# Optimization experiments

Measured on AMD Instinct MI355X. Metric: run time of the kernel, lower is better.

The kernel has to match this reference:

```python
import jax, jax.numpy as jnp
import numpy as np

COMMITMENT_COST = 0.25
LAMBDA_KL = 1.0
EPS = 1e-10


def setup_inputs() -> dict:
    key = jax.random.key(0)
    k1, k2 = jax.random.split(key)
    x = jax.random.normal(k1, (8, 4096, 256), dtype=jnp.float32)
    embedding = jax.random.normal(k2, (1024, 256), dtype=jnp.float32)
    return {"x": x, "embedding": embedding}


def reference(x, embedding):
    B, T, D = x.shape
    M, _ = embedding.shape
    x_sg = jax.lax.stop_gradient(x)
    x_flat = x_sg.reshape(-1, D)  # [N, D]
    distances = (jnp.sum(embedding ** 2, axis=1)[None, :]
                 + jnp.sum(x_flat ** 2, axis=1, keepdims=True)
                 - 2.0 * (x_flat @ embedding.T))  # [N, M]
    indices = jnp.argmin(distances.astype(jnp.float32), axis=-1)  # [N]
    quantized = embedding[indices].reshape(B, T, D)
    # losses (x detached in both terms, matching torch)
    loss = (COMMITMENT_COST * jnp.mean((x_sg - quantized) ** 2)
            + jnp.mean((quantized - x_sg) ** 2)) * LAMBDA_KL
    # straight-through estimator
    quantized_st = x + jax.lax.stop_gradient(quantized - x)
    # avg of one-hot encodings == normalized code counts (avoids NxM one-hot)
    N = B * T
    counts = jnp.zeros((M,), dtype=jnp.float32).at[indices].add(1.0)
    avg_probs = counts / N
    perplexity = jnp.exp(-jnp.sum(avg_probs * jnp.log(avg_probs + EPS)))
    return (quantized_st, loss, indices.reshape(B, T), perplexity)
```

## Files before the change

### kernel.cpp

```cpp
#include <hip/hip_runtime.h>


constexpr int D = 256;
constexpr int M = 1024;
constexpr int ROWS = 64;

typedef _Float16 f16;
typedef __attribute__((ext_vector_type(8))) _Float16 f16x8;
typedef __attribute__((ext_vector_type(4))) float f32x4;

constexpr size_t WS_ENORM_F = 1028;
constexpr size_t WS_TAB_B   = 8320;
constexpr size_t WS_NEEDED  = 1056896;

__device__ inline void gload_lds16(const void* g, void* l) {
    __builtin_amdgcn_global_load_lds(
        (const __attribute__((address_space(1))) unsigned int*)(g),
        (__attribute__((address_space(3))) unsigned int*)(l), 16, 0, 0);
}

__global__ __launch_bounds__(256) void prep_kernel(const float* __restrict__ e,
                                                   float* __restrict__ ws) {
    const int b = blockIdx.x, t = threadIdx.x;
    if (b < 256) {
        int v    = b * 256 + t;
        int lane = v & 63, unit = v >> 6;
        int rf = unit & 1, spl = (unit >> 1) & 1, kk = (unit >> 2) & 7, tile = unit >> 5;
        int lr = lane & 15, q = lane >> 4;
        const float* p = e + (size_t)(tile * 32 + rf * 16 + lr) * D + kk * 32 + q * 8;
        f32x4 a = *reinterpret_cast<const f32x4*>(p);
        f32x4 c = *reinterpret_cast<const f32x4*>(p + 4);
        f16 h0=(f16)a.x,h1=(f16)a.y,h2=(f16)a.z,h3=(f16)a.w;
        f16 h4=(f16)c.x,h5=(f16)c.y,h6=(f16)c.z,h7=(f16)c.w;
        f16x8 out;
        if (spl == 0) out = (f16x8){h0,h1,h2,h3,h4,h5,h6,h7};
        else          out = (f16x8){(f16)(a.x-(float)h0),(f16)(a.y-(float)h1),
                                    (f16)(a.z-(float)h2),(f16)(a.w-(float)h3),
                                    (f16)(c.x-(float)h4),(f16)(c.y-(float)h5),
                                    (f16)(c.z-(float)h6),(f16)(c.w-(float)h7)};
        *reinterpret_cast<f16x8*>((char*)ws + WS_TAB_B + (size_t)v * 16) = out;
    } else {
        int row  = (b - 256) * 4 + (t >> 6);
        int lane = t & 63;
        f32x4 a = *reinterpret_cast<const f32x4*>(e + (size_t)row * D + lane * 4);
        float s = fmaf(a.x, a.x, fmaf(a.y, a.y, fmaf(a.z, a.z, a.w * a.w)));
#pragma unroll
        for (int o = 32; o > 0; o >>= 1) s += __shfl_down(s, o, 64);
        if (lane == 0) ws[WS_ENORM_F + row] = s;
    }
}

__global__ __launch_bounds__(256, 2) void vq_fused_kernel(
    const float* __restrict__ x, const float* __restrict__ e,
    float* __restrict__ outQ, float* __restrict__ outIdx, float* __restrict__ ws)
{
    __shared__ ushort ebuf[2][16384];
    __shared__ float  en_s[M];
    __shared__ int    fidx[ROWS];
    __shared__ float  lsum[4];

    const int tid = threadIdx.x;
    const int w   = __builtin_amdgcn_readfirstlane(tid >> 6);
    const int l   = tid & 63;
    const int lr  = l & 15, q = l >> 4;
    const int R   = blockIdx.x * ROWS;
    const char* tab = (const char*)ws + WS_TAB_B;

    {
        f32x4 v = *reinterpret_cast<const f32x4*>(ws + WS_ENORM_F + tid * 4);
        *reinterpret_cast<f32x4*>(&en_s[tid * 4]) = v;
    }

    f16x8 Xh[8], Xl[8];
    float xn;
    {
        float s = 0.f;
#pragma unroll
        for (int kk = 0; kk < 8; ++kk) {
            const float* p = x + (size_t)(R + w * 16 + lr) * D + kk * 32 + q * 8;
            f32x4 a = *reinterpret_cast<const f32x4*>(p);
            f32x4 c = *reinterpret_cast<const f32x4*>(p + 4);
            f16 h0=(f16)a.x,h1=(f16)a.y,h2=(f16)a.z,h3=(f16)a.w;
            f16 h4=(f16)c.x,h5=(f16)c.y,h6=(f16)c.z,h7=(f16)c.w;
            Xh[kk] = (f16x8){h0,h1,h2,h3,h4,h5,h6,h7};
            Xl[kk] = (f16x8){(f16)(a.x-(float)h0),(f16)(a.y-(float)h1),
                             (f16)(a.z-(float)h2),(f16)(a.w-(float)h3),
                             (f16)(c.x-(float)h4),(f16)(c.y-(float)h5),
                             (f16)(c.z-(float)h6),(f16)(c.w-(float)h7)};
            s = fmaf(a.x,a.x,fmaf(a.y,a.y,fmaf(a.z,a.z,fmaf(a.w,a.w,
                fmaf(c.x,c.x,fmaf(c.y,c.y,fmaf(c.z,c.z,fmaf(c.w,c.w,s))))))));
        }
        s += __shfl_xor(s, 16, 64);
        s += __shfl_xor(s, 32, 64);
        xn = s;
    }

#pragma unroll
    for (int i = 0; i < 8; ++i)
        gload_lds16(tab + (w * 8 + i) * 1024 + l * 16, &ebuf[0][(w * 8 + i) * 512]);
    __syncthreads();

    float bV = 3.4e38f;
    int   bI = 0;

    for (int t = 0; t < 32; ++t) {
        const ushort* eb = &ebuf[t & 1][0];
        if (t < 31) {
            const char* gt = tab + (size_t)(t + 1) * 32768;
            ushort* lb = &ebuf[(t + 1) & 1][0];
#pragma unroll
            for (int i = 0; i < 8; ++i)
                gload_lds16(gt + (w * 8 + i) * 1024 + l * 16, lb + (w * 8 + i) * 512);
        }

        f32x4 accA[2], accB[2];
#pragma unroll
        for (int rf = 0; rf < 2; ++rf) {
            accA[rf] = (f32x4){0.f,0.f,0.f,0.f};
            accB[rf] = (f32x4){0.f,0.f,0.f,0.f};
        }
#pragma unroll
        for (int kk = 0; kk < 8; ++kk) {
            f16x8 Ah0 = *reinterpret_cast<const f16x8*>(eb + (kk*4+0)*512 + l*8);
            f16x8 Ah1 = *reinterpret_cast<const f16x8*>(eb + (kk*4+1)*512 + l*8);
            f16x8 Al0 = *reinterpret_cast<const f16x8*>(eb + (kk*4+2)*512 + l*8);
            f16x8 Al1 = *reinterpret_cast<const f16x8*>(eb + (kk*4+3)*512 + l*8);
            accA[0] = __builtin_amdgcn_mfma_f32_16x16x32_f16(Ah0, Xh[kk], accA[0], 0, 0, 0);
            accA[0] = __builtin_amdgcn_mfma_f32_16x16x32_f16(Ah0, Xl[kk], accA[0], 0, 0, 0);
            accB[0] = __builtin_amdgcn_mfma_f32_16x16x32_f16(Al0, Xh[kk], accB[0], 0, 0, 0);
            accA[1] = __builtin_amdgcn_mfma_f32_16x16x32_f16(Ah1, Xh[kk], accA[1], 0, 0, 0);
            accA[1] = __builtin_amdgcn_mfma_f32_16x16x32_f16(Ah1, Xl[kk], accA[1], 0, 0, 0);
            accB[1] = __builtin_amdgcn_mfma_f32_16x16x32_f16(Al1, Xh[kk], accB[1], 0, 0, 0);
        }
        __syncthreads();

#pragma unroll
        for (int rf = 0; rf < 2; ++rf) {
            f32x4 en4 = *reinterpret_cast<const f32x4*>(&en_s[t * 32 + rf * 16 + q * 4]);
#pragma unroll
            for (int i = 0; i < 4; ++i) {
                float dv = fmaf(-2.f, accA[rf][i] + accB[rf][i], en4[i]);
                int   mi = t * 32 + rf * 16 + q * 4 + i;
                if (dv < bV) { bV = dv; bI = mi; }
            }
        }
    }

#pragma unroll
    for (int mk = 16; mk <= 32; mk <<= 1) {
        float ov = __shfl_xor(bV, mk, 64);
        int   oi = __shfl_xor(bI, mk, 64);
        if (ov < bV || (ov == bV && oi < bI)) { bV = ov; bI = oi; }
    }
    if (q == 0) {
        fidx[w * 16 + lr] = bI;
        outIdx[R + w * 16 + lr] = (float)bI;
        atomicAdd(ws + 1 + bI, 1.0f);
        float ls = bV + xn;
#pragma unroll
        for (int o = 8; o > 0; o >>= 1) ls += __shfl_down(ls, o, 64);
        if (lr == 0) lsum[w] = ls;
    }
    __syncthreads();
    if (tid == 0) atomicAdd(ws, lsum[0] + lsum[1] + lsum[2] + lsum[3]);

#pragma unroll
    for (int it = 0; it < 16; ++it) {
        int u = it * 256 + tid;
        int row = u >> 6, c4 = u & 63;
        f32x4 v = *reinterpret_cast<const f32x4*>(e + (size_t)fidx[row] * D + c4 * 4);
        __builtin_nontemporal_store(v, reinterpret_cast<f32x4*>(outQ + (size_t)(R + row) * D + c4 * 4));
    }
}

__global__ void enorm_kernel(const float* __restrict__ e, float* __restrict__ enorm) {
    int m = blockIdx.x, l = threadIdx.x;
    const f32x4 v = *reinterpret_cast<const f32x4*>(e + m * D + l * 4);
    float s = fmaf(v.x, v.x, fmaf(v.y, v.y, fmaf(v.z, v.z, v.w * v.w)));
#pragma unroll
    for (int o = 32; o > 0; o >>= 1) s += __shfl_down(s, o, 64);
    if (l == 0) enorm[m] = s;
}

__global__ __launch_bounds__(256, 2) void vq_main_kernel(
    const float* __restrict__ x, const float* __restrict__ e,
    float* __restrict__ outQ, float* __restrict__ outIdx, float* __restrict__ ws) {
    __shared__ f32x4 xs[64][64];
    __shared__ float cval[4][64];
    __shared__ int   cidx[4][64];
    __shared__ int   fidx[64];
    const int tid = threadIdx.x, row0 = blockIdx.x * 64;
#pragma unroll
    for (int it = 0; it < 16; ++it) {
        int f = it * 256 + tid, rr = f >> 6, c4 = f & 63;
        xs[rr][c4 ^ (rr & 7)] = *reinterpret_cast<const f32x4*>(x + (row0 + rr) * D + c4 * 4);
    }
    __syncthreads();
    const int r = tid & 63, c = __builtin_amdgcn_readfirstlane(tid >> 6), sw = r & 7;
    float xnorm = 0.f;
    if (c == 0) {
        f32x4 a = (f32x4){0.f,0.f,0.f,0.f};
        for (int d4 = 0; d4 < 64; ++d4) {
            f32x4 xv = xs[r][d4 ^ sw];
            a.x = fmaf(xv.x, xv.x, a.x); a.y = fmaf(xv.y, xv.y, a.y);
            a.z = fmaf(xv.z, xv.z, a.z); a.w = fmaf(xv.w, xv.w, a.w);
        }
        xnorm = (a.x + a.y) + (a.z + a.w);
    }
    const float* __restrict__ enorm = ws + WS_ENORM_F;
    float bestVal = 3.4e38f; int bestIdx = 0;
    for (int chunk = 0; chunk < M / 32; ++chunk) {
        const int m0 = chunk * 32 + c * 8;
        f32x4 acc[8];
#pragma unroll
        for (int mi = 0; mi < 8; ++mi) acc[mi] = (f32x4){0.f,0.f,0.f,0.f};
#pragma unroll 2
        for (int d4 = 0; d4 < 64; ++d4) {
            const f32x4 xv = xs[r][d4 ^ sw];
#pragma unroll
            for (int mi = 0; mi < 8; ++mi) {
                const f32x4 ev = *reinterpret_cast<const f32x4*>(e + (m0 + mi) * D + d4 * 4);
                acc[mi].x = fmaf(xv.x, ev.x, acc[mi].x); acc[mi].y = fmaf(xv.y, ev.y, acc[mi].y);
                acc[mi].z = fmaf(xv.z, ev.z, acc[mi].z); acc[mi].w = fmaf(xv.w, ev.w, acc[mi].w);
            }
        }
#pragma unroll
        for (int mi = 0; mi < 8; ++mi) {
            float dot = (acc[mi].x + acc[mi].y) + (acc[mi].z + acc[mi].w);
            float val = enorm[m0 + mi] - 2.0f * dot;
            if (val < bestVal) { bestVal = val; bestIdx = m0 + mi; }
        }
    }
    cval[c][r] = bestVal; cidx[c][r] = bestIdx;
    __syncthreads();
    if (c == 0) {
        float bv = bestVal; int bi = bestIdx;
#pragma unroll
        for (int cc = 1; cc < 4; ++cc) {
            float v = cval[cc][r]; int i = cidx[cc][r];
            if (v < bv || (v == bv && i < bi)) { bv = v; bi = i; }
        }
        fidx[r] = bi; outIdx[row0 + r] = (float)bi;
        atomicAdd(ws + 1 + bi, 1.0f);
        float dist = bv + xnorm;
#pragma unroll
        for (int o = 32; o > 0; o >>= 1) dist += __shfl_down(dist, o, 64);
        if (r == 0) atomicAdd(ws, dist);
    }
    __syncthreads();
#pragma unroll
    for (int it = 0; it < 16; ++it) {
        int f = it * 256 + tid, rr = f >> 6, c4 = f & 63;
        *reinterpret_cast<f32x4*>(outQ + (row0 + rr) * D + c4 * 4) =
            *reinterpret_cast<const f32x4*>(e + fidx[rr] * D + c4 * 4);
    }
}

__global__ void vq_final_kernel(const float* __restrict__ ws,
                                float* __restrict__ outLoss, float* __restrict__ outPpl,
                                float invN, float invND) {
    int t = threadIdx.x;
    float p = ws[1 + t] * invN;
    float term = p * logf(p + 1e-10f);
#pragma unroll
    for (int o = 32; o > 0; o >>= 1) term += __shfl_down(term, o, 64);
    __shared__ float s[16];
    if ((t & 63) == 0) s[t >> 6] = term;
    __syncthreads();
    if (t == 0) {
        float tot = 0.f;
#pragma unroll
        for (int i = 0; i < 16; ++i) tot += s[i];
        *outPpl  = expf(-tot);
        *outLoss = 1.25f * ws[0] * invND;
    }
}

extern "C" void kernel_launch(void* const* d_in, const int* in_sizes, int n_in,
                              void* d_out, int out_size, void* d_ws, size_t ws_size,
                              hipStream_t stream) {
    const float* x = (const float*)d_in[0];
    const float* e = (const float*)d_in[1];
    const int NX = in_sizes[0];
    const int N  = NX / D;

    float* out     = (float*)d_out;
    float* outQ    = out;
    float* outLoss = out + NX;
    float* outIdx  = out + NX + 1;
    float* outPpl  = out + NX + 1 + N;
    float* ws      = (float*)d_ws;

    (void)hipMemsetAsync(d_ws, 0, 4100, stream);
    if (ws_size >= WS_NEEDED && (N % ROWS) == 0) {
        prep_kernel<<<512, 256, 0, stream>>>(e, ws);
        vq_fused_kernel<<<N / ROWS, 256, 0, stream>>>(x, e, outQ, outIdx, ws);
    } else {
        enorm_kernel<<<M, 64, 0, stream>>>(e, ws + WS_ENORM_F);
        vq_main_kernel<<<N / 64, 256, 0, stream>>>(x, e, outQ, outIdx, ws);
    }
    vq_final_kernel<<<1, 1024, 0, stream>>>(ws, outLoss, outPpl,
                                            1.0f / (float)N, 1.0f / (float)NX);
}
```

Measured before the change: 89.38 us.

## Switch codebook staging to triple-buffered 16-code tiles with single barrier

Reorganizes the fp16 hi/lo codebook table into 16-code tiles and streams it through a three-deep LDS ring. Each iteration issues one explicit vmcnt wait and one barrier instead of two __syncthreads, and prefetches two tiles ahead. MFMA sections are raised with s_setprio so their issue is favored. Per-iteration work is halved (one 16x16 tile), which doubles loop iterations and barrier count, and correctness now depends on hand-written waitcnt values matching the number of outstanding loads.

Result: slower. 100.2 us (+12.1%).

```diff
diff --git a/kernel.cpp b/kernel.cpp
--- a/kernel.cpp
+++ b/kernel.cpp
@@ -25,9 +25,9 @@
     if (b < 256) {
         int v    = b * 256 + t;
         int lane = v & 63, unit = v >> 6;
-        int rf = unit & 1, spl = (unit >> 1) & 1, kk = (unit >> 2) & 7, tile = unit >> 5;
+        int spl = unit & 1, kk = (unit >> 1) & 7, t16 = unit >> 4;
         int lr = lane & 15, q = lane >> 4;
-        const float* p = e + (size_t)(tile * 32 + rf * 16 + lr) * D + kk * 32 + q * 8;
+        const float* p = e + (size_t)(t16 * 16 + lr) * D + kk * 32 + q * 8;
         f32x4 a = *reinterpret_cast<const f32x4*>(p);
         f32x4 c = *reinterpret_cast<const f32x4*>(p + 4);
         f16 h0=(f16)a.x,h1=(f16)a.y,h2=(f16)a.z,h3=(f16)a.w;
@@ -54,7 +54,7 @@
     const float* __restrict__ x, const float* __restrict__ e,
     float* __restrict__ outQ, float* __restrict__ outIdx, float* __restrict__ ws)
 {
-    __shared__ ushort ebuf[2][16384];
+    __shared__ ushort ebuf[3][8192];
     __shared__ float  en_s[M];
     __shared__ int    fidx[ROWS];
     __shared__ float  lsum[4];
@@ -65,6 +65,15 @@
     const int lr  = l & 15, q = l >> 4;
     const int R   = blockIdx.x * ROWS;
     const char* tab = (const char*)ws + WS_TAB_B;
+
+    auto stage = [&](int buf, int g) {
+#pragma unroll
+        for (int i = 0; i < 4; ++i) {
+            int sg = w * 4 + i;
+            gload_lds16(tab + (size_t)g * 16384 + sg * 1024 + l * 16,
+                        &ebuf[buf][sg * 512]);
+        }
+    };
 
     {
         f32x4 v = *reinterpret_cast<const f32x4*>(ws + WS_ENORM_F + tid * 4);
@@ -95,55 +104,48 @@
         xn = s;
     }
 
-#pragma unroll
-    for (int i = 0; i < 8; ++i)
-        gload_lds16(tab + (w * 8 + i) * 1024 + l * 16, &ebuf[0][(w * 8 + i) * 512]);
-    __syncthreads();
+    __builtin_amdgcn_sched_barrier(0);
+    stage(0, 0);
+    stage(1, 1);
+    asm volatile("s_waitcnt lgkmcnt(0)" ::: "memory");
 
     float bV = 3.4e38f;
     int   bI = 0;
-
-    for (int t = 0; t < 32; ++t) {
-        const ushort* eb = &ebuf[t & 1][0];
-        if (t < 31) {
-            const char* gt = tab + (size_t)(t + 1) * 32768;
-            ushort* lb = &ebuf[(t + 1) & 1][0];
-#pragma unroll
-            for (int i = 0; i < 8; ++i)
-                gload_lds16(gt + (w * 8 + i) * 1024 + l * 16, lb + (w * 8 + i) * 512);
-        }
-
-        f32x4 accA[2], accB[2];
-#pragma unroll
-        for (int rf = 0; rf < 2; ++rf) {
-            accA[rf] = (f32x4){0.f,0.f,0.f,0.f};
-            accB[rf] = (f32x4){0.f,0.f,0.f,0.f};
-        }
+    int   cb = 0;
+
+    for (int g = 0; g < 64; ++g) {
+        if (g < 63) asm volatile("s_waitcnt vmcnt(4)" ::: "memory");
+        else        asm volatile("s_waitcnt vmcnt(0)" ::: "memory");
+        __builtin_amdgcn_s_barrier();
+
+        if (g + 2 < 64) {
+            int pb = cb + 2; if (pb >= 3) pb -= 3;
+            stage(pb, g + 2);
+        }
+
+        const ushort* eb = &ebuf[cb][0];
+        f32x4 accA = (f32x4){0.f,0.f,0.f,0.f};
+        f32x4 accB = (f32x4){0.f,0.f,0.f,0.f};
+        __builtin_amdgcn_s_setprio(1);
 #pragma unroll
         for (int kk = 0; kk < 8; ++kk) {
-            f16x8 Ah0 = *reinterpret_cast<const f16x8*>(eb + (kk*4+0)*512 + l*8);
-            f16x8 Ah1 = *reinterpret_cast<const f16x8*>(eb + (kk*4+1)*512 + l*8);
-            f16x8 Al0 = *reinterpret_cast<const f16x8*>(eb + (kk*4+2)*512 + l*8);
-            f16x8 Al1 = *reinterpret_cast<const f16x8*>(eb + (kk*4+3)*512 + l*8);
-            accA[0] = __builtin_amdgcn_mfma_f32_16x16x32_f16(Ah0, Xh[kk], accA[0], 0, 0, 0);
-            accA[0] = __builtin_amdgcn_mfma_f32_16x16x32_f16(Ah0, Xl[kk], accA[0], 0, 0, 0);
-            accB[0] = __builtin_amdgcn_mfma_f32_16x16x32_f16(Al0, Xh[kk], accB[0], 0, 0, 0);
-            accA[1] = __builtin_amdgcn_mfma_f32_16x16x32_f16(Ah1, Xh[kk], accA[1], 0, 0, 0);
-            accA[1] = __builtin_amdgcn_mfma_f32_16x16x32_f16(Ah1, Xl[kk], accA[1], 0, 0, 0);
-            accB[1] = __builtin_amdgcn_mfma_f32_16x16x32_f16(Al1, Xh[kk], accB[1], 0, 0, 0);
-        }
-        __syncthreads();
-
-#pragma unroll
-        for (int rf = 0; rf < 2; ++rf) {
-            f32x4 en4 = *reinterpret_cast<const f32x4*>(&en_s[t * 32 + rf * 16 + q * 4]);
-#pragma unroll
-            for (int i = 0; i < 4; ++i) {
-                float dv = fmaf(-2.f, accA[rf][i] + accB[rf][i], en4[i]);
-                int   mi = t * 32 + rf * 16 + q * 4 + i;
-                if (dv < bV) { bV = dv; bI = mi; }
-            }
-        }
+            f16x8 Ah = *reinterpret_cast<const f16x8*>(eb + (kk*2+0)*512 + l*8);
+            f16x8 Al = *reinterpret_cast<const f16x8*>(eb + (kk*2+1)*512 + l*8);
+            accA = __builtin_amdgcn_mfma_f32_16x16x32_f16(Ah, Xh[kk], accA, 0, 0, 0);
+            accA = __builtin_amdgcn_mfma_f32_16x16x32_f16(Ah, Xl[kk], accA, 0, 0, 0);
+            accB = __builtin_amdgcn_mfma_f32_16x16x32_f16(Al, Xh[kk], accB, 0, 0, 0);
+        }
+        __builtin_amdgcn_s_setprio(0);
+
+        const int mbase = g * 16;
+        f32x4 en4 = *reinterpret_cast<const f32x4*>(&en_s[mbase + q * 4]);
+#pragma unroll
+        for (int i = 0; i < 4; ++i) {
+            float dv = fmaf(-2.f, accA[i] + accB[i], en4[i]);
+            int   mi = mbase + q * 4 + i;
+            if (dv < bV) { bV = dv; bI = mi; }
+        }
+        cb = cb + 1; if (cb >= 3) cb -= 3;
     }
 
 #pragma unroll
@@ -153,12 +155,13 @@
         if (ov < bV || (ov == bV && oi < bI)) { bV = ov; bI = oi; }
     }
     if (q == 0) {
-        fidx[w * 16 + lr] = bI;
-        outIdx[R + w * 16 + lr] = (float)bI;
+        int r = w * 16 + lr;
+        fidx[r] = bI;
+        outIdx[R + r] = (float)bI;
         atomicAdd(ws + 1 + bI, 1.0f);
         float ls = bV + xn;
 #pragma unroll
-        for (int o = 8; o > 0; o >>= 1) ls += __shfl_down(ls, o, 64);
+        for (int o = 8; o > 0; o >>= 1) ls += __shfl_down(ls, o, 16);
         if (lr == 0) lsum[w] = ls;
     }
     __syncthreads();
```
